# Kernel optimization log

Hardware: AMD Instinct MI355X
Metric: run time of the kernel (lower is better)

The kernel has to match this reference:

```python
import jax, jax.numpy as jnp
import numpy as np

# Model dims (match init_kwargs)
X = 256   # input_size
H = 512   # num_units
R = 128   # r_size
M = 128   # mem_cap
TAU = 1.0
F_BIAS = 1.0
T = 256   # timesteps
B = 256   # batch


def setup_inputs() -> dict:
    key = jax.random.key(0)
    ks = jax.random.split(key, 10)
    return {
        "x": jax.random.normal(ks[0], (T, B, X), jnp.float32),
        "noise": jax.random.uniform(ks[1], (T, B, M), jnp.float32),
        "W_full": jax.random.normal(ks[2], (X + R + H, R + 4 * H), jnp.float32) * 0.05,
        "bias": jnp.zeros((R + 4 * H,), jnp.float32),
        "W_full1": jax.random.normal(ks[3], (X + R + H, R + H), jnp.float32) * 0.05,
        "bias1": jnp.zeros((R + H,), jnp.float32),
        "fc_w": jax.random.normal(ks[4], (M, X + H), jnp.float32) * 0.05,
        "fc_b": jnp.zeros((M,), jnp.float32),
        "trans_w": jax.random.normal(ks[5], (R, H), jnp.float32) * 0.05,
        "trans_b": jnp.zeros((R,), jnp.float32),
        "c_bias": jax.random.normal(ks[6], (1, H), jnp.float32),
        "hmem_bias": jnp.zeros((1, M, R), jnp.float32),
    }


def _armin_scan(x, noise, W_full, bias, W_full1, bias1, fc_w, fc_b,
                trans_w, trans_b, c_bias, hmem_bias):
    c0 = jnp.tanh(jnp.broadcast_to(c_bias, (B, H)))
    hmem0 = jnp.broadcast_to(hmem_bias, (B, M, R)) + jnp.zeros((B, M, R), x.dtype)

    def step(carry, inp):
        c, hmem = carry
        x_t, g_t, t = inp
        # read head: fc([x, c]) -> [B, M]
        head = jnp.concatenate([x_t, c], axis=1) @ fc_w.T + fc_b
        # gumbel-softmax with straight-through hard one-hot
        gumbel = -jnp.log(1e-20 - jnp.log(1e-20 + g_t))
        y = jax.nn.softmax((head + gumbel) * TAU, axis=1)
        hard = jax.nn.one_hot(jnp.argmax(y, axis=1), M, dtype=y.dtype)
        h_index = jax.lax.stop_gradient(hard - y) + y          # [B, M]
        h_entry = jnp.einsum('bm,bmr->br', h_index, hmem)      # memory read [B, R]
        # gated cell
        concat = jnp.concatenate([x_t, c, h_entry], axis=1)    # [B, X+H+R]
        gates1 = jax.nn.sigmoid(concat @ W_full1 + bias1)      # [B, R+H]
        concat = concat * jnp.concatenate([jnp.ones_like(x_t), gates1], axis=1)
        pre = concat @ W_full + bias                           # [B, R+4H]
        i, j, f, o = pre[:, :H], pre[:, H:2*H], pre[:, 2*H:3*H], pre[:, 3*H:4*H]
        om = pre[:, 4*H:]                                      # [B, R] (remainder chunk)
        new_c = jnp.tanh(c * jax.nn.sigmoid(f + F_BIAS)
                         + jax.nn.sigmoid(i) * jnp.tanh(j))
        new_h = new_c * jax.nn.sigmoid(o)
        r = h_entry * jax.nn.sigmoid(om)
        # write: sequential fill while memcnt < mem_cap, else last read slot
        fill = jax.nn.one_hot(t, M, dtype=y.dtype)[None, :]
        w_idx = jnp.where(t < M, fill, jax.lax.stop_gradient(h_index))[..., None]
        wv = new_c @ trans_w.T + trans_b                       # [B, R]
        hmem = wv[:, None, :] * w_idx + hmem * (1.0 - w_idx)
        return (new_c, hmem), jnp.concatenate([new_h, r], axis=1)

    (_, _), outs = jax.lax.scan(step, (c0, hmem0), (x, noise, jnp.arange(T)))
    return outs  # [T, B, H+R]


def reference(x, noise, W_full, bias, W_full1, bias1, fc_w, fc_b,
              trans_w, trans_b, c_bias, hmem_bias):
    return _armin_scan(x, noise, W_full, bias, W_full1, bias1, fc_w, fc_b,
                       trans_w, trans_b, c_bias, hmem_bias)
```

## Files before the change

kernel.cpp:

```cpp
#include <hip/hip_runtime.h>
#include <cmath>


#define TT 256
#define BB 256
#define XD 256
#define HD 512
#define RD 128
#define MD 128
#define N1 640
#define NP 2176

#define OFF_C     0u
#define OFF_HMEM  131072u
#define OFF_HENT  4325376u
#define OFF_SEL   4358144u
#define OFF_FXT   4358400u
#define OFF_TWT   4391168u
#define OFF_FWT   4456704u
#define OFF_HEAD0 4522240u
#define OFF_G1P   4522496u
#define OFF_PREP  4850176u

__device__ __forceinline__ float sigm(float z){ return 1.0f/(1.0f + expf(-z)); }
__device__ __forceinline__ float4 ld4(const float* p){ return *(const float4*)p; }

__global__ __launch_bounds__(256)
void k_pre(const float* __restrict__ fc_w, const float* __restrict__ trans_w,
           const float* __restrict__ c_bias, const float* __restrict__ hmem_bias,
           float* __restrict__ ws)
{
  float*  cbuf   = ws + OFF_C;
  float*  hmem   = ws + OFF_HMEM;
  float*  fcxT   = ws + OFF_FXT;
  float*  transT = ws + OFF_TWT;
  float*  fcwcT  = ws + OFF_FWT;
  double* head0d = (double*)(ws + OFF_HEAD0);

  const int gt = blockIdx.x*256 + threadIdx.x, GT = gridDim.x*256;
  for (int i = gt; i < BB*HD;    i += GT) cbuf[i] = (float)tanh((double)c_bias[i & 511]);
  for (int i = gt; i < BB*MD*RD; i += GT) hmem[i] = hmem_bias[i & (MD*RD - 1)];
  for (int i = gt; i < XD*128;   i += GT) { int k=i>>7, m=i&127; fcxT[i]  = fc_w[(size_t)m*768 + k]; }
  for (int i = gt; i < HD*128;   i += GT) { int k=i>>7, o=i&127; transT[i] = trans_w[(size_t)o*512 + k];
                                            fcwcT[i]  = fc_w[(size_t)o*768 + 256 + k]; }
  if (blockIdx.x == 0 && threadIdx.x < 128) {
    double a = 0.0;
    for (int k = 0; k < 512; ++k)
      a += tanh((double)c_bias[k]) * (double)fc_w[(size_t)threadIdx.x*768 + 256 + k];
    head0d[threadIdx.x] = a;
  }
}

__global__ __launch_bounds__(256)
void k_score(const float* __restrict__ x, const float* __restrict__ noise,
             const float* __restrict__ fc_b, const float* __restrict__ ws_fcxT,
             float* __restrict__ out)
{
  __shared__ float xs[16*256];
  const int tid = threadIdx.x;
  const int rbase = blockIdx.x * 16;
  for (int i = tid; i < 16*64; i += 256) {
    int row = i >> 6, kq = (i & 63) << 2;
    *(float4*)&xs[row*256 + kq] = ld4(x + (size_t)(rbase + row)*XD + kq);
  }
  __syncthreads();
  const int m = tid & 127, r0 = (tid >> 7) * 8;
  double acc[8] = {};
  for (int k = 0; k < 256; ++k) {
    double wk = (double)ws_fcxT[k*128 + m];
    #pragma unroll
    for (int r = 0; r < 8; ++r) acc[r] += wk * (double)xs[(r0+r)*256 + k];
  }
  #pragma unroll
  for (int r = 0; r < 8; ++r) {
    size_t grow = (size_t)rbase + r0 + r;
    double g   = (double)noise[grow*MD + m];
    double gum = -log(1e-20 - log(1e-20 + g));
    out[grow*640 + 512 + m] = (float)(acc[r] + (double)fc_b[m] + gum);
  }
}

__global__ __launch_bounds__(256)
void k_gates1(const float* __restrict__ x, const float* __restrict__ W_full1,
              const float* __restrict__ out, float* __restrict__ ws, int t)
{
  __shared__ float As[16][68];
  __shared__ float Bs[16][64];
  __shared__ int   sel[64];
  const int tid = threadIdx.x, bid = blockIdx.x;
  const int rt = bid & 3, ct = (bid >> 2) % 10, kc = bid / 40;
  const int r0 = rt*64, n0 = ct*64, kbeg = kc*448;
  const float* cbuf = ws + OFF_C;
  const float* hmem = ws + OFF_HMEM;
  float*  hent  = ws + OFF_HENT;
  int*    selb  = (int*)(ws + OFF_SEL);
  double* head0d= (double*)(ws + OFF_HEAD0);
  float*  g1p   = ws + OFF_G1P + (size_t)kc*BB*N1;

  if (kc == 1) {
    if (tid < 64) {
      const float* sc = out + ((size_t)t*BB + r0 + tid)*640 + 512;
      int bi = 0;
      if (t == 0) { double best = -1e300;
        for (int m = 0; m < 128; ++m) { double v = (double)sc[m] + head0d[m]; if (v > best) { best = v; bi = m; } } }
      else { float best = -3.4e38f;
        for (int m = 0; m < 128; ++m) { float v = sc[m]; if (v > best) { best = v; bi = m; } } }
      sel[tid] = bi;
    }
    __syncthreads();
    if (ct == 0) {
      if (tid < 64) selb[r0 + tid] = sel[tid];
      for (int idx = tid; idx < 64*128; idx += 256) {
        int row = idx >> 7, rr = idx & 127;
        hent[(size_t)(r0+row)*RD + rr] = hmem[((size_t)(r0+row)*MD + sel[row])*RD + rr];
      }
    }
  }

  float  acc[4][4] = {};
  double accd[4][4] = {};
  const int tx = tid & 15, ty = tid >> 4;
  const int arow = tid >> 2, akq = (tid & 3) << 2;
  const int bkk = tid >> 4, bnq = (tid & 15) << 2;

  for (int k0 = kbeg; k0 < kbeg + 448; k0 += 16) {
    __syncthreads();
    {
      int b = r0 + arow, k = k0 + akq;
      float4 v;
      if (k < XD)           v = ld4(x + ((size_t)t*BB + b)*XD + k);
      else if (k < XD + HD) v = ld4(cbuf + (size_t)b*HD + (k - XD));
      else                  v = ld4(hmem + ((size_t)b*MD + sel[arow])*RD + (k - (XD+HD)));
      As[akq+0][arow] = v.x; As[akq+1][arow] = v.y;
      As[akq+2][arow] = v.z; As[akq+3][arow] = v.w;
    }
    *(float4*)&Bs[bkk][bnq] = ld4(W_full1 + (size_t)(k0 + bkk)*N1 + n0 + bnq);
    __syncthreads();
    #pragma unroll
    for (int kk = 0; kk < 16; ++kk) {
      float a[4], b[4];
      *(float4*)a = ld4(&As[kk][ty*4]);
      *(float4*)b = ld4(&Bs[kk][tx*4]);
      #pragma unroll
      for (int i = 0; i < 4; ++i)
        #pragma unroll
        for (int j = 0; j < 4; ++j)
          acc[i][j] = fmaf(a[i], b[j], acc[i][j]);
      if ((kk & 7) == 7) {
        #pragma unroll
        for (int i = 0; i < 4; ++i)
          #pragma unroll
          for (int j = 0; j < 4; ++j) { accd[i][j] += (double)acc[i][j]; acc[i][j] = 0.f; }
      }
    }
  }
  #pragma unroll
  for (int i = 0; i < 4; ++i)
    #pragma unroll
    for (int j = 0; j < 4; ++j)
      g1p[(size_t)(r0 + ty*4 + i)*N1 + n0 + tx*4 + j] = (float)accd[i][j];
}

__global__ __launch_bounds__(256)
void k_pre_gemm(const float* __restrict__ x, const float* __restrict__ W_full,
                const float* __restrict__ bias1, float* __restrict__ ws, int t)
{
  __shared__ float As[16][68];
  __shared__ float Bs[16][128];
  const int tid = threadIdx.x, bid = blockIdx.x;
  const int rt = bid & 3, ct = (bid >> 2) % 17, kc = bid / 68;
  const int r0 = rt*64, n0 = ct*128, kbeg = kc*448;
  const float* cbuf = ws + OFF_C;
  const float* hent = ws + OFF_HENT;
  const float* g1p0 = ws + OFF_G1P;
  const float* g1p1 = g1p0 + (size_t)BB*N1;
  float* prep = ws + OFF_PREP + (size_t)kc*BB*NP;

  float  acc[4][8] = {};
  double accd[4][8] = {};
  const int tx = tid & 15, ty = tid >> 4;
  const int arow = tid >> 2, akq = (tid & 3) << 2;

  for (int k0 = kbeg; k0 < kbeg + 448; k0 += 16) {
    __syncthreads();
    {
      int b = r0 + arow, k = k0 + akq;
      float4 v;
      if (k < XD) v = ld4(x + ((size_t)t*BB + b)*XD + k);
      else if (k < XD + HD) {
        int j = k - XD;
        v = ld4(cbuf + (size_t)b*HD + j);
        float4 p0 = ld4(g1p0 + (size_t)b*N1 + j);
        float4 p1 = ld4(g1p1 + (size_t)b*N1 + j);
        float4 bb = ld4(bias1 + j);
        v.x *= sigm(p0.x + p1.x + bb.x);
        v.y *= sigm(p0.y + p1.y + bb.y);
        v.z *= sigm(p0.z + p1.z + bb.z);
        v.w *= sigm(p0.w + p1.w + bb.w);
      } else {
        int j = k - (XD + HD);
        v = ld4(hent + (size_t)b*RD + j);
        float4 p0 = ld4(g1p0 + (size_t)b*N1 + 512 + j);
        float4 p1 = ld4(g1p1 + (size_t)b*N1 + 512 + j);
        float4 bb = ld4(bias1 + 512 + j);
        v.x *= sigm(p0.x + p1.x + bb.x);
        v.y *= sigm(p0.y + p1.y + bb.y);
        v.z *= sigm(p0.z + p1.z + bb.z);
        v.w *= sigm(p0.w + p1.w + bb.w);
      }
      As[akq+0][arow] = v.x; As[akq+1][arow] = v.y;
      As[akq+2][arow] = v.z; As[akq+3][arow] = v.w;
    }
    #pragma unroll
    for (int rep = 0; rep < 2; ++rep) {
      int idx = tid + rep*256, kk = idx >> 5, nq = (idx & 31) << 2;
      *(float4*)&Bs[kk][nq] = ld4(W_full + (size_t)(k0 + kk)*NP + n0 + nq);
    }
    __syncthreads();
    #pragma unroll
    for (int kk = 0; kk < 16; ++kk) {
      float a[4], b[8];
      *(float4*)a = ld4(&As[kk][ty*4]);
      *(float4*)&b[0] = ld4(&Bs[kk][tx*8]);
      *(float4*)&b[4] = ld4(&Bs[kk][tx*8 + 4]);
      #pragma unroll
      for (int i = 0; i < 4; ++i)
        #pragma unroll
        for (int j = 0; j < 8; ++j)
          acc[i][j] = fmaf(a[i], b[j], acc[i][j]);
      if ((kk & 7) == 7) {
        #pragma unroll
        for (int i = 0; i < 4; ++i)
          #pragma unroll
          for (int j = 0; j < 8; ++j) { accd[i][j] += (double)acc[i][j]; acc[i][j] = 0.f; }
      }
    }
  }
  #pragma unroll
  for (int i = 0; i < 4; ++i)
    #pragma unroll
    for (int j = 0; j < 8; ++j)
      prep[(size_t)(r0 + ty*4 + i)*NP + n0 + tx*8 + j] = (float)accd[i][j];
}

__global__ __launch_bounds__(256)
void k_epi(const float* __restrict__ bias, const float* __restrict__ trans_b,
           float* __restrict__ out, float* __restrict__ ws, int t)
{
  __shared__ float smc[4*512];
  __shared__ float smwv[4*128];
  const int tid = threadIdx.x, b0 = blockIdx.x*4;
  float*  cbuf   = ws + OFF_C;
  float*  hmem   = ws + OFF_HMEM;
  float*  hent   = ws + OFF_HENT;
  int*    selb   = (int*)(ws + OFF_SEL);
  float*  transT = ws + OFF_TWT;
  float*  fcwcT  = ws + OFF_FWT;
  const float* prep0 = ws + OFF_PREP;
  const float* prep1 = prep0 + (size_t)BB*NP;

  for (int idx = tid; idx < 4*512; idx += 256) {
    int br = idx >> 9, hh = idx & 511, b = b0 + br;
    const float* p0 = prep0 + (size_t)b*NP;
    const float* p1 = prep1 + (size_t)b*NP;
    float iv = p0[hh]        + p1[hh]        + bias[hh];
    float jv = p0[512 + hh]  + p1[512 + hh]  + bias[512 + hh];
    float fv = p0[1024 + hh] + p1[1024 + hh] + bias[1024 + hh];
    float ov = p0[1536 + hh] + p1[1536 + hh] + bias[1536 + hh];
    float cold = cbuf[(size_t)b*HD + hh];
    float nc = tanhf(cold*sigm(fv + 1.0f) + sigm(iv)*tanhf(jv));
    cbuf[(size_t)b*HD + hh] = nc;
    smc[br*512 + hh] = nc;
    out[((size_t)t*BB + b)*640 + hh] = nc * sigm(ov);
  }
  for (int idx = tid; idx < 4*128; idx += 256) {
    int br = idx >> 7, rr = idx & 127, b = b0 + br;
    float om = prep0[(size_t)b*NP + 2048 + rr] + prep1[(size_t)b*NP + 2048 + rr] + bias[2048 + rr];
    out[((size_t)t*BB + b)*640 + 512 + rr] = hent[(size_t)b*RD + rr] * sigm(om);
  }
  __syncthreads();
  if (t < TT-1) {
    int o = tid & 127, mat = tid >> 7;
    const float* WT = mat ? fcwcT : transT;
    double a0=0., a1=0., a2=0., a3=0.;
    for (int k = 0; k < 512; k += 4) {
      float w0 = WT[(k+0)*128 + o], w1 = WT[(k+1)*128 + o];
      float w2 = WT[(k+2)*128 + o], w3 = WT[(k+3)*128 + o];
      float4 c0v = ld4(&smc[0*512 + k]);
      float4 c1v = ld4(&smc[1*512 + k]);
      float4 c2v = ld4(&smc[2*512 + k]);
      float4 c3v = ld4(&smc[3*512 + k]);
      a0 += (double)w0*c0v.x + (double)w1*c0v.y + (double)w2*c0v.z + (double)w3*c0v.w;
      a1 += (double)w0*c1v.x + (double)w1*c1v.y + (double)w2*c1v.z + (double)w3*c1v.w;
      a2 += (double)w0*c2v.x + (double)w1*c2v.y + (double)w2*c2v.z + (double)w3*c2v.w;
      a3 += (double)w0*c3v.x + (double)w1*c3v.y + (double)w2*c3v.z + (double)w3*c3v.w;
    }
    if (mat == 0) {
      smwv[0*128+o] = (float)(a0 + (double)trans_b[o]);
      smwv[1*128+o] = (float)(a1 + (double)trans_b[o]);
      smwv[2*128+o] = (float)(a2 + (double)trans_b[o]);
      smwv[3*128+o] = (float)(a3 + (double)trans_b[o]);
    } else {
      float* sx = out + ((size_t)(t+1)*BB)*640;
      sx[(size_t)(b0+0)*640 + 512 + o] = (float)((double)sx[(size_t)(b0+0)*640 + 512 + o] + a0);
      sx[(size_t)(b0+1)*640 + 512 + o] = (float)((double)sx[(size_t)(b0+1)*640 + 512 + o] + a1);
      sx[(size_t)(b0+2)*640 + 512 + o] = (float)((double)sx[(size_t)(b0+2)*640 + 512 + o] + a2);
      sx[(size_t)(b0+3)*640 + 512 + o] = (float)((double)sx[(size_t)(b0+3)*640 + 512 + o] + a3);
    }
    __syncthreads();
    for (int idx = tid; idx < 4*128; idx += 256) {
      int br = idx >> 7, rr = idx & 127, b = b0 + br;
      int slot = (t < MD) ? t : selb[b];
      hmem[((size_t)b*MD + slot)*RD + rr] = smwv[br*128 + rr];
    }
  }
}

extern "C" void kernel_launch(void* const* d_in, const int* in_sizes, int n_in,
                              void* d_out, int out_size, void* d_ws, size_t ws_size,
                              hipStream_t stream) {
  const float* x         = (const float*)d_in[0];
  const float* noise     = (const float*)d_in[1];
  const float* W_full    = (const float*)d_in[2];
  const float* bias      = (const float*)d_in[3];
  const float* W_full1   = (const float*)d_in[4];
  const float* bias1     = (const float*)d_in[5];
  const float* fc_w      = (const float*)d_in[6];
  const float* fc_b      = (const float*)d_in[7];
  const float* trans_w   = (const float*)d_in[8];
  const float* trans_b   = (const float*)d_in[9];
  const float* c_bias    = (const float*)d_in[10];
  const float* hmem_bias = (const float*)d_in[11];
  float* out = (float*)d_out;
  float* ws  = (float*)d_ws;

  k_pre  <<<dim3(256),  dim3(256), 0, stream>>>(fc_w, trans_w, c_bias, hmem_bias, ws);
  k_score<<<dim3(4096), dim3(256), 0, stream>>>(x, noise, fc_b, ws + OFF_FXT, out);
  for (int t = 0; t < TT; ++t) {
    k_gates1  <<<dim3(80),  dim3(256), 0, stream>>>(x, W_full1, out, ws, t);
    k_pre_gemm<<<dim3(136), dim3(256), 0, stream>>>(x, W_full, bias1, ws, t);
    k_epi     <<<dim3(64),  dim3(256), 0, stream>>>(bias, trans_b, out, ws, t);
  }
}
```

Measured before the change: 38.20 ms.

## Fuse per-timestep kernels into one persistent kernel with grid barriers

Replaces the 768 per-timestep launches (three kernels per step) with a single persistent kernel of 136 blocks. The blocks loop over all timesteps and separate the gates1, pre-GEMM and epilogue phases with a software grid barrier built on an atomic counter. This removes kernel launch and inter-kernel gap overhead, at the cost of spin-wait barriers. It also adds a timeout abort path that silently returns if the blocks are not all co-resident.

```diff
diff --git a/kernel.cpp b/kernel.cpp
--- a/kernel.cpp
+++ b/kernel.cpp
@@ -21,6 +21,11 @@
 #define OFF_HEAD0 4522240u
 #define OFF_G1P   4522496u
 #define OFF_PREP  4850176u
+
+#define NBLK 136
+
+__device__ unsigned int g_cnt;
+__device__ unsigned int g_abrt;
 
 __device__ __forceinline__ float sigm(float z){ return 1.0f/(1.0f + expf(-z)); }
 __device__ __forceinline__ float4 ld4(const float* p){ return *(const float4*)p; }
@@ -38,6 +43,7 @@
   double* head0d = (double*)(ws + OFF_HEAD0);
 
   const int gt = blockIdx.x*256 + threadIdx.x, GT = gridDim.x*256;
+  if (gt == 0) { g_cnt = 0u; g_abrt = 0u; }
   for (int i = gt; i < BB*HD;    i += GT) cbuf[i] = (float)tanh((double)c_bias[i & 511]);
   for (int i = gt; i < BB*MD*RD; i += GT) hmem[i] = hmem_bias[i & (MD*RD - 1)];
   for (int i = gt; i < XD*128;   i += GT) { int k=i>>7, m=i&127; fcxT[i]  = fc_w[(size_t)m*768 + k]; }
@@ -81,238 +87,266 @@
 }
 
 __global__ __launch_bounds__(256)
-void k_gates1(const float* __restrict__ x, const float* __restrict__ W_full1,
-              const float* __restrict__ out, float* __restrict__ ws, int t)
-{
-  __shared__ float As[16][68];
-  __shared__ float Bs[16][64];
-  __shared__ int   sel[64];
-  const int tid = threadIdx.x, bid = blockIdx.x;
-  const int rt = bid & 3, ct = (bid >> 2) % 10, kc = bid / 40;
-  const int r0 = rt*64, n0 = ct*64, kbeg = kc*448;
-  const float* cbuf = ws + OFF_C;
-  const float* hmem = ws + OFF_HMEM;
-  float*  hent  = ws + OFF_HENT;
-  int*    selb  = (int*)(ws + OFF_SEL);
-  double* head0d= (double*)(ws + OFF_HEAD0);
-  float*  g1p   = ws + OFF_G1P + (size_t)kc*BB*N1;
-
-  if (kc == 1) {
-    if (tid < 64) {
-      const float* sc = out + ((size_t)t*BB + r0 + tid)*640 + 512;
-      int bi = 0;
-      if (t == 0) { double best = -1e300;
-        for (int m = 0; m < 128; ++m) { double v = (double)sc[m] + head0d[m]; if (v > best) { best = v; bi = m; } } }
-      else { float best = -3.4e38f;
-        for (int m = 0; m < 128; ++m) { float v = sc[m]; if (v > best) { best = v; bi = m; } } }
-      sel[tid] = bi;
-    }
-    __syncthreads();
-    if (ct == 0) {
-      if (tid < 64) selb[r0 + tid] = sel[tid];
-      for (int idx = tid; idx < 64*128; idx += 256) {
-        int row = idx >> 7, rr = idx & 127;
-        hent[(size_t)(r0+row)*RD + rr] = hmem[((size_t)(r0+row)*MD + sel[row])*RD + rr];
-      }
-    }
-  }
-
-  float  acc[4][4] = {};
-  double accd[4][4] = {};
-  const int tx = tid & 15, ty = tid >> 4;
-  const int arow = tid >> 2, akq = (tid & 3) << 2;
-  const int bkk = tid >> 4, bnq = (tid & 15) << 2;
-
-  for (int k0 = kbeg; k0 < kbeg + 448; k0 += 16) {
-    __syncthreads();
-    {
-      int b = r0 + arow, k = k0 + akq;
-      float4 v;
-      if (k < XD)           v = ld4(x + ((size_t)t*BB + b)*XD + k);
-      else if (k < XD + HD) v = ld4(cbuf + (size_t)b*HD + (k - XD));
-      else                  v = ld4(hmem + ((size_t)b*MD + sel[arow])*RD + (k - (XD+HD)));
-      As[akq+0][arow] = v.x; As[akq+1][arow] = v.y;
-      As[akq+2][arow] = v.z; As[akq+3][arow] = v.w;
-    }
-    *(float4*)&Bs[bkk][bnq] = ld4(W_full1 + (size_t)(k0 + bkk)*N1 + n0 + bnq);
-    __syncthreads();
-    #pragma unroll
-    for (int kk = 0; kk < 16; ++kk) {
-      float a[4], b[4];
-      *(float4*)a = ld4(&As[kk][ty*4]);
-      *(float4*)b = ld4(&Bs[kk][tx*4]);
-      #pragma unroll
-      for (int i = 0; i < 4; ++i)
-        #pragma unroll
-        for (int j = 0; j < 4; ++j)
-          acc[i][j] = fmaf(a[i], b[j], acc[i][j]);
-      if ((kk & 7) == 7) {
-        #pragma unroll
-        for (int i = 0; i < 4; ++i)
-          #pragma unroll
-          for (int j = 0; j < 4; ++j) { accd[i][j] += (double)acc[i][j]; acc[i][j] = 0.f; }
-      }
-    }
-  }
-  #pragma unroll
-  for (int i = 0; i < 4; ++i)
-    #pragma unroll
-    for (int j = 0; j < 4; ++j)
-      g1p[(size_t)(r0 + ty*4 + i)*N1 + n0 + tx*4 + j] = (float)accd[i][j];
-}
-
-__global__ __launch_bounds__(256)
-void k_pre_gemm(const float* __restrict__ x, const float* __restrict__ W_full,
-                const float* __restrict__ bias1, float* __restrict__ ws, int t)
+void k_scan(const float* __restrict__ x, const float* __restrict__ W_full,
+            const float* __restrict__ W_full1, const float* __restrict__ bias,
+            const float* __restrict__ bias1, const float* __restrict__ trans_b,
+            float* __restrict__ out, float* __restrict__ ws)
 {
   __shared__ float As[16][68];
   __shared__ float Bs[16][128];
+  __shared__ int   sel[64];
+  __shared__ float smc[4*512];
+  __shared__ float smwv[4*128];
+  __shared__ int   s_bad;
+
   const int tid = threadIdx.x, bid = blockIdx.x;
-  const int rt = bid & 3, ct = (bid >> 2) % 17, kc = bid / 68;
-  const int r0 = rt*64, n0 = ct*128, kbeg = kc*448;
-  const float* cbuf = ws + OFF_C;
-  const float* hent = ws + OFF_HENT;
-  const float* g1p0 = ws + OFF_G1P;
-  const float* g1p1 = g1p0 + (size_t)BB*N1;
-  float* prep = ws + OFF_PREP + (size_t)kc*BB*NP;
-
-  float  acc[4][8] = {};
-  double accd[4][8] = {};
-  const int tx = tid & 15, ty = tid >> 4;
-  const int arow = tid >> 2, akq = (tid & 3) << 2;
-
-  for (int k0 = kbeg; k0 < kbeg + 448; k0 += 16) {
+  unsigned int bars = 0;
+
+  auto gbar = [&]() -> bool {
+    ++bars;
+    const unsigned int target = (unsigned int)NBLK * bars;
     __syncthreads();
-    {
-      int b = r0 + arow, k = k0 + akq;
-      float4 v;
-      if (k < XD) v = ld4(x + ((size_t)t*BB + b)*XD + k);
-      else if (k < XD + HD) {
-        int j = k - XD;
-        v = ld4(cbuf + (size_t)b*HD + j);
-        float4 p0 = ld4(g1p0 + (size_t)b*N1 + j);
-        float4 p1 = ld4(g1p1 + (size_t)b*N1 + j);
-        float4 bb = ld4(bias1 + j);
-        v.x *= sigm(p0.x + p1.x + bb.x);
-        v.y *= sigm(p0.y + p1.y + bb.y);
-        v.z *= sigm(p0.z + p1.z + bb.z);
-        v.w *= sigm(p0.w + p1.w + bb.w);
-      } else {
-        int j = k - (XD + HD);
-        v = ld4(hent + (size_t)b*RD + j);
-        float4 p0 = ld4(g1p0 + (size_t)b*N1 + 512 + j);
-        float4 p1 = ld4(g1p1 + (size_t)b*N1 + 512 + j);
-        float4 bb = ld4(bias1 + 512 + j);
-        v.x *= sigm(p0.x + p1.x + bb.x);
-        v.y *= sigm(p0.y + p1.y + bb.y);
-        v.z *= sigm(p0.z + p1.z + bb.z);
-        v.w *= sigm(p0.w + p1.w + bb.w);
-      }
-      As[akq+0][arow] = v.x; As[akq+1][arow] = v.y;
-      As[akq+2][arow] = v.z; As[akq+3][arow] = v.w;
-    }
-    #pragma unroll
-    for (int rep = 0; rep < 2; ++rep) {
-      int idx = tid + rep*256, kk = idx >> 5, nq = (idx & 31) << 2;
-      *(float4*)&Bs[kk][nq] = ld4(W_full + (size_t)(k0 + kk)*NP + n0 + nq);
+    if (tid == 0) {
+      __threadfence();
+      __hip_atomic_fetch_add(&g_cnt, 1u, __ATOMIC_RELEASE, __HIP_MEMORY_SCOPE_AGENT);
+      long long t0 = __builtin_amdgcn_s_memrealtime();
+      int bad = 0;
+      while (__hip_atomic_load(&g_cnt, __ATOMIC_ACQUIRE, __HIP_MEMORY_SCOPE_AGENT) < target) {
+        __builtin_amdgcn_s_sleep(8);
+        if (__hip_atomic_load(&g_abrt, __ATOMIC_RELAXED, __HIP_MEMORY_SCOPE_AGENT) != 0u) { bad = 1; break; }
+        if (__builtin_amdgcn_s_memrealtime() - t0 > 5000000LL) {
+          __hip_atomic_store(&g_abrt, 1u, __ATOMIC_RELAXED, __HIP_MEMORY_SCOPE_AGENT);
+          bad = 1; break;
+        }
+      }
+      __threadfence();
+      s_bad = bad;
     }
     __syncthreads();
-    #pragma unroll
-    for (int kk = 0; kk < 16; ++kk) {
-      float a[4], b[8];
-      *(float4*)a = ld4(&As[kk][ty*4]);
-      *(float4*)&b[0] = ld4(&Bs[kk][tx*8]);
-      *(float4*)&b[4] = ld4(&Bs[kk][tx*8 + 4]);
+    return s_bad == 0;
+  };
+
+  for (int t = 0; t < TT; ++t) {
+    if (bid < 80) {
+      const int rt = bid & 3, ct = (bid >> 2) % 10, kc = bid / 40;
+      const int r0 = rt*64, n0 = ct*64, kbeg = kc*448;
+      const float* cbuf = ws + OFF_C;
+      const float* hmem = ws + OFF_HMEM;
+      float*  hent  = ws + OFF_HENT;
+      int*    selb  = (int*)(ws + OFF_SEL);
+      double* head0d= (double*)(ws + OFF_HEAD0);
+      float*  g1p   = ws + OFF_G1P + (size_t)kc*BB*N1;
+
+      if (kc == 1) {
+        if (tid < 64) {
+          const float* sc = out + ((size_t)t*BB + r0 + tid)*640 + 512;
+          int bi = 0;
+          if (t == 0) { double best = -1e300;
+            for (int m = 0; m < 128; ++m) { double v = (double)sc[m] + head0d[m]; if (v > best) { best = v; bi = m; } } }
+          else { float best = -3.4e38f;
+            for (int m = 0; m < 128; ++m) { float v = sc[m]; if (v > best) { best = v; bi = m; } } }
+          sel[tid] = bi;
+        }
+        __syncthreads();
+        if (ct == 0) {
+          if (tid < 64) selb[r0 + tid] = sel[tid];
+          for (int idx = tid; idx < 64*128; idx += 256) {
+            int row = idx >> 7, rr = idx & 127;
+            hent[(size_t)(r0+row)*RD + rr] = hmem[((size_t)(r0+row)*MD + sel[row])*RD + rr];
+          }
+        }
+      }
+
+      float  acc[4][4] = {};
+      double accd[4][4] = {};
+      const int tx = tid & 15, ty = tid >> 4;
+      const int arow = tid >> 2, akq = (tid & 3) << 2;
+      const int bkk = tid >> 4, bnq = (tid & 15) << 2;
+
+      for (int k0 = kbeg; k0 < kbeg + 448; k0 += 16) {
+        __syncthreads();
+        {
+          int b = r0 + arow, k = k0 + akq;
+          float4 v;
+          if (k < XD)           v = ld4(x + ((size_t)t*BB + b)*XD + k);
+          else if (k < XD + HD) v = ld4(cbuf + (size_t)b*HD + (k - XD));
+          else                  v = ld4(hmem + ((size_t)b*MD + sel[arow])*RD + (k - (XD+HD)));
+          As[akq+0][arow] = v.x; As[akq+1][arow] = v.y;
+          As[akq+2][arow] = v.z; As[akq+3][arow] = v.w;
+        }
+        *(float4*)&Bs[bkk][bnq] = ld4(W_full1 + (size_t)(k0 + bkk)*N1 + n0 + bnq);
+        __syncthreads();
+        #pragma unroll
+        for (int kk = 0; kk < 16; ++kk) {
+          float a[4], b[4];
+          *(float4*)a = ld4(&As[kk][ty*4]);
+          *(float4*)b = ld4(&Bs[kk][tx*4]);
+          #pragma unroll
+          for (int i = 0; i < 4; ++i)
+            #pragma unroll
+            for (int j = 0; j < 4; ++j)
+              acc[i][j] = fmaf(a[i], b[j], acc[i][j]);
+          if ((kk & 7) == 7) {
+            #pragma unroll
+            for (int i = 0; i < 4; ++i)
+              #pragma unroll
+              for (int j = 0; j < 4; ++j) { accd[i][j] += (double)acc[i][j]; acc[i][j] = 0.f; }
+          }
+        }
+      }
       #pragma unroll
       for (int i = 0; i < 4; ++i)
         #pragma unroll
+        for (int j = 0; j < 4; ++j)
+          g1p[(size_t)(r0 + ty*4 + i)*N1 + n0 + tx*4 + j] = (float)accd[i][j];
+    }
+    if (!gbar()) return;
+
+    {
+      const int rt = bid & 3, ct = (bid >> 2) % 17, kc = bid / 68;
+      const int r0 = rt*64, n0 = ct*128, kbeg = kc*448;
+      const float* cbuf = ws + OFF_C;
+      const float* hent = ws + OFF_HENT;
+      const float* g1p0 = ws + OFF_G1P;
+      const float* g1p1 = g1p0 + (size_t)BB*N1;
+      float* prep = ws + OFF_PREP + (size_t)kc*BB*NP;
+
+      float  acc[4][8] = {};
+      double accd[4][8] = {};
+      const int tx = tid & 15, ty = tid >> 4;
+      const int arow = tid >> 2, akq = (tid & 3) << 2;
+
+      for (int k0 = kbeg; k0 < kbeg + 448; k0 += 16) {
+        __syncthreads();
+        {
+          int b = r0 + arow, k = k0 + akq;
+          float4 v;
+          if (k < XD) v = ld4(x + ((size_t)t*BB + b)*XD + k);
+          else if (k < XD + HD) {
+            int j = k - XD;
+            v = ld4(cbuf + (size_t)b*HD + j);
+            float4 p0 = ld4(g1p0 + (size_t)b*N1 + j);
+            float4 p1 = ld4(g1p1 + (size_t)b*N1 + j);
+            float4 bb = ld4(bias1 + j);
+            v.x *= sigm(p0.x + p1.x + bb.x);
+            v.y *= sigm(p0.y + p1.y + bb.y);
+            v.z *= sigm(p0.z + p1.z + bb.z);
+            v.w *= sigm(p0.w + p1.w + bb.w);
+          } else {
+            int j = k - (XD + HD);
+            v = ld4(hent + (size_t)b*RD + j);
+            float4 p0 = ld4(g1p0 + (size_t)b*N1 + 512 + j);
+            float4 p1 = ld4(g1p1 + (size_t)b*N1 + 512 + j);
+            float4 bb = ld4(bias1 + 512 + j);
+            v.x *= sigm(p0.x + p1.x + bb.x);
+            v.y *= sigm(p0.y + p1.y + bb.y);
+            v.z *= sigm(p0.z + p1.z + bb.z);
+            v.w *= sigm(p0.w + p1.w + bb.w);
+          }
+          As[akq+0][arow] = v.x; As[akq+1][arow] = v.y;
+          As[akq+2][arow] = v.z; As[akq+3][arow] = v.w;
+        }
+        #pragma unroll
+        for (int rep = 0; rep < 2; ++rep) {
+          int idx = tid + rep*256, kk = idx >> 5, nq = (idx & 31) << 2;
+          *(float4*)&Bs[kk][nq] = ld4(W_full + (size_t)(k0 + kk)*NP + n0 + nq);
+        }
+        __syncthreads();
+        #pragma unroll
+        for (int kk = 0; kk < 16; ++kk) {
+          float a[4], b[8];
+          *(float4*)a = ld4(&As[kk][ty*4]);
+          *(float4*)&b[0] = ld4(&Bs[kk][tx*8]);
+          *(float4*)&b[4] = ld4(&Bs[kk][tx*8 + 4]);
+          #pragma unroll
+          for (int i = 0; i < 4; ++i)
+            #pragma unroll
+            for (int j = 0; j < 8; ++j)
+              acc[i][j] = fmaf(a[i], b[j], acc[i][j]);
+          if ((kk & 7) == 7) {
+            #pragma unroll
+            for (int i = 0; i < 4; ++i)
+              #pragma unroll
+              for (int j = 0; j < 8; ++j) { accd[i][j] += (double)acc[i][j]; acc[i][j] = 0.f; }
+          }
+        }
+      }
+      #pragma unroll
+      for (int i = 0; i < 4; ++i)
+        #pragma unroll
         for (int j = 0; j < 8; ++j)
-          acc[i][j] = fmaf(a[i], b[j], acc[i][j]);
-      if ((kk & 7) == 7) {
-        #pragma unroll
-        for (int i = 0; i < 4; ++i)
-          #pragma unroll
-          for (int j = 0; j < 8; ++j) { accd[i][j] += (double)acc[i][j]; acc[i][j] = 0.f; }
-      }
+          prep[(size_t)(r0 + ty*4 + i)*NP + n0 + tx*8 + j] = (float)accd[i][j];
     }
-  }
-  #pragma unroll
-  for (int i = 0; i < 4; ++i)
-    #pragma unroll
-    for (int j = 0; j < 8; ++j)
-      prep[(size_t)(r0 + ty*4 + i)*NP + n0 + tx*8 + j] = (float)accd[i][j];
-}
-
-__global__ __launch_bounds__(256)
-void k_epi(const float* __restrict__ bias, const float* __restrict__ trans_b,
-           float* __restrict__ out, float* __restrict__ ws, int t)
-{
-  __shared__ float smc[4*512];
-  __shared__ float smwv[4*128];
-  const int tid = threadIdx.x, b0 = blockIdx.x*4;
-  float*  cbuf   = ws + OFF_C;
-  float*  hmem   = ws + OFF_HMEM;
-  float*  hent   = ws + OFF_HENT;
-  int*    selb   = (int*)(ws + OFF_SEL);
-  float*  transT = ws + OFF_TWT;
-  float*  fcwcT  = ws + OFF_FWT;
-  const float* prep0 = ws + OFF_PREP;
-  const float* prep1 = prep0 + (size_t)BB*NP;
-
-  for (int idx = tid; idx < 4*512; idx += 256) {
-    int br = idx >> 9, hh = idx & 511, b = b0 + br;
-    const float* p0 = prep0 + (size_t)b*NP;
-    const float* p1 = prep1 + (size_t)b*NP;
-    float iv = p0[hh]        + p1[hh]        + bias[hh];
-    float jv = p0[512 + hh]  + p1[512 + hh]  + bias[512 + hh];
-    float fv = p0[1024 + hh] + p1[1024 + hh] + bias[1024 + hh];
-    float ov = p0[1536 + hh] + p1[1536 + hh] + bias[1536 + hh];
-    float cold = cbuf[(size_t)b*HD + hh];
-    float nc = tanhf(cold*sigm(fv + 1.0f) + sigm(iv)*tanhf(jv));
-    cbuf[(size_t)b*HD + hh] = nc;
-    smc[br*512 + hh] = nc;
-    out[((size_t)t*BB + b)*640 + hh] = nc * sigm(ov);
-  }
-  for (int idx = tid; idx < 4*128; idx += 256) {
-    int br = idx >> 7, rr = idx & 127, b = b0 + br;
-    float om = prep0[(size_t)b*NP + 2048 + rr] + prep1[(size_t)b*NP + 2048 + rr] + bias[2048 + rr];
-    out[((size_t)t*BB + b)*640 + 512 + rr] = hent[(size_t)b*RD + rr] * sigm(om);
-  }
-  __syncthreads();
-  if (t < TT-1) {
-    int o = tid & 127, mat = tid >> 7;
-    const float* WT = mat ? fcwcT : transT;
-    double a0=0., a1=0., a2=0., a3=0.;
-    for (int k = 0; k < 512; k += 4) {
-      float w0 = WT[(k+0)*128 + o], w1 = WT[(k+1)*128 + o];
-      float w2 = WT[(k+2)*128 + o], w3 = WT[(k+3)*128 + o];
-      float4 c0v = ld4(&smc[0*512 + k]);
-      float4 c1v = ld4(&smc[1*512 + k]);
-      float4 c2v = ld4(&smc[2*512 + k]);
-      float4 c3v = ld4(&smc[3*512 + k]);
-      a0 += (double)w0*c0v.x + (double)w1*c0v.y + (double)w2*c0v.z + (double)w3*c0v.w;
-      a1 += (double)w0*c1v.x + (double)w1*c1v.y + (double)w2*c1v.z + (double)w3*c1v.w;
-      a2 += (double)w0*c2v.x + (double)w1*c2v.y + (double)w2*c2v.z + (double)w3*c2v.w;
-      a3 += (double)w0*c3v.x + (double)w1*c3v.y + (double)w2*c3v.z + (double)w3*c3v.w;
+    if (!gbar()) return;
+
+    if (bid < 64) {
+      const int b0 = bid*4;
+      float*  cbuf   = ws + OFF_C;
+      float*  hmem   = ws + OFF_HMEM;
+      float*  hent   = ws + OFF_HENT;
+      int*    selb   = (int*)(ws + OFF_SEL);
+      float*  transT = ws + OFF_TWT;
+      float*  fcwcT  = ws + OFF_FWT;
+      const float* prep0 = ws + OFF_PREP;
+      const float* prep1 = prep0 + (size_t)BB*NP;
+
+      for (int idx = tid; idx < 4*512; idx += 256) {
+        int br = idx >> 9, hh = idx & 511, b = b0 + br;
+        const float* p0 = prep0 + (size_t)b*NP;
+        const float* p1 = prep1 + (size_t)b*NP;
+        float iv = p0[hh]        + p1[hh]        + bias[hh];
+        float jv = p0[512 + hh]  + p1[512 + hh]  + bias[512 + hh];
+        float fv = p0[1024 + hh] + p1[1024 + hh] + bias[1024 + hh];
+        float ov = p0[1536 + hh] + p1[1536 + hh] + bias[1536 + hh];
+        float cold = cbuf[(size_t)b*HD + hh];
+        float nc = tanhf(cold*sigm(fv + 1.0f) + sigm(iv)*tanhf(jv));
+        cbuf[(size_t)b*HD + hh] = nc;
+        smc[br*512 + hh] = nc;
+        out[((size_t)t*BB + b)*640 + hh] = nc * sigm(ov);
+      }
+      for (int idx = tid; idx < 4*128; idx += 256) {
+        int br = idx >> 7, rr = idx & 127, b = b0 + br;
+        float om = prep0[(size_t)b*NP + 2048 + rr] + prep1[(size_t)b*NP + 2048 + rr] + bias[2048 + rr];
+        out[((size_t)t*BB + b)*640 + 512 + rr] = hent[(size_t)b*RD + rr] * sigm(om);
+      }
+      __syncthreads();
+      if (t < TT-1) {
+        int o = tid & 127, mat = tid >> 7;
+        const float* WT = mat ? fcwcT : transT;
+        double a0=0., a1=0., a2=0., a3=0.;
+        for (int k = 0; k < 512; k += 4) {
+          float w0 = WT[(k+0)*128 + o], w1 = WT[(k+1)*128 + o];
+          float w2 = WT[(k+2)*128 + o], w3 = WT[(k+3)*128 + o];
+          float4 c0v = ld4(&smc[0*512 + k]);
+          float4 c1v = ld4(&smc[1*512 + k]);
+          float4 c2v = ld4(&smc[2*512 + k]);
+          float4 c3v = ld4(&smc[3*512 + k]);
+          a0 += (double)w0*c0v.x + (double)w1*c0v.y + (double)w2*c0v.z + (double)w3*c0v.w;
+          a1 += (double)w0*c1v.x + (double)w1*c1v.y + (double)w2*c1v.z + (double)w3*c1v.w;
+          a2 += (double)w0*c2v.x + (double)w1*c2v.y + (double)w2*c2v.z + (double)w3*c2v.w;
+          a3 += (double)w0*c3v.x + (double)w1*c3v.y + (double)w2*c3v.z + (double)w3*c3v.w;
+        }
+        if (mat == 0) {
+          smwv[0*128+o] = (float)(a0 + (double)trans_b[o]);
+          smwv[1*128+o] = (float)(a1 + (double)trans_b[o]);
+          smwv[2*128+o] = (float)(a2 + (double)trans_b[o]);
+          smwv[3*128+o] = (float)(a3 + (double)trans_b[o]);
+        } else {
+          float* sx = out + ((size_t)(t+1)*BB)*640;
+          sx[(size_t)(b0+0)*640 + 512 + o] = (float)((double)sx[(size_t)(b0+0)*640 + 512 + o] + a0);
+          sx[(size_t)(b0+1)*640 + 512 + o] = (float)((double)sx[(size_t)(b0+1)*640 + 512 + o] + a1);
+          sx[(size_t)(b0+2)*640 + 512 + o] = (float)((double)sx[(size_t)(b0+2)*640 + 512 + o] + a2);
+          sx[(size_t)(b0+3)*640 + 512 + o] = (float)((double)sx[(size_t)(b0+3)*640 + 512 + o] + a3);
+        }
+        __syncthreads();
+        for (int idx = tid; idx < 4*128; idx += 256) {
+          int br = idx >> 7, rr = idx & 127, b = b0 + br;
+          int slot = (t < MD) ? t : selb[b];
+          hmem[((size_t)b*MD + slot)*RD + rr] = smwv[br*128 + rr];
+        }
+      }
     }
-    if (mat == 0) {
-      smwv[0*128+o] = (float)(a0 + (double)trans_b[o]);
-      smwv[1*128+o] = (float)(a1 + (double)trans_b[o]);
-      smwv[2*128+o] = (float)(a2 + (double)trans_b[o]);
-      smwv[3*128+o] = (float)(a3 + (double)trans_b[o]);
-    } else {
-      float* sx = out + ((size_t)(t+1)*BB)*640;
-      sx[(size_t)(b0+0)*640 + 512 + o] = (float)((double)sx[(size_t)(b0+0)*640 + 512 + o] + a0);
-      sx[(size_t)(b0+1)*640 + 512 + o] = (float)((double)sx[(size_t)(b0+1)*640 + 512 + o] + a1);
-      sx[(size_t)(b0+2)*640 + 512 + o] = (float)((double)sx[(size_t)(b0+2)*640 + 512 + o] + a2);
-      sx[(size_t)(b0+3)*640 + 512 + o] = (float)((double)sx[(size_t)(b0+3)*640 + 512 + o] + a3);
-    }
-    __syncthreads();
-    for (int idx = tid; idx < 4*128; idx += 256) {
-      int br = idx >> 7, rr = idx & 127, b = b0 + br;
-      int slot = (t < MD) ? t : selb[b];
-      hmem[((size_t)b*MD + slot)*RD + rr] = smwv[br*128 + rr];
-    }
+    if (!gbar()) return;
   }
 }
 
@@ -336,9 +370,6 @@
 
   k_pre  <<<dim3(256),  dim3(256), 0, stream>>>(fc_w, trans_w, c_bias, hmem_bias, ws);
   k_score<<<dim3(4096), dim3(256), 0, stream>>>(x, noise, fc_b, ws + OFF_FXT, out);
-  for (int t = 0; t < TT; ++t) {
-    k_gates1  <<<dim3(80),  dim3(256), 0, stream>>>(x, W_full1, out, ws, t);
-    k_pre_gemm<<<dim3(136), dim3(256), 0, stream>>>(x, W_full, bias1, ws, t);
-    k_epi     <<<dim3(64),  dim3(256), 0, stream>>>(bias, trans_b, out, ws, t);
-  }
+  k_scan <<<dim3(NBLK), dim3(256), 0, stream>>>(x, W_full, W_full1, bias, bias1,
+                                                trans_b, out, ws);
 }
```

After: 56.03 ms. +46.7%, slower.
